# Performance work log

Hardware: AMD Instinct MI355X
Metric: run time of the kernel (lower is better)

## Reference

```python
import jax, jax.numpy as jnp
import numpy as np

N = 262144
IN_DIM = 1024
HID = 256
E = 16
TOP_K = 2


def setup_inputs() -> dict:
    key = jax.random.key(0)
    k1, k2, k3, k4, k5 = jax.random.split(key, 5)
    x = jax.random.normal(k1, (N, IN_DIM), dtype=jnp.float32)
    # Kaiming-ish init scaled for stability
    W1 = jax.random.normal(k2, (IN_DIM, HID), dtype=jnp.float32) * (1.0 / np.sqrt(IN_DIM))
    b1 = jnp.zeros((HID,), dtype=jnp.float32)
    W2 = jax.random.normal(k3, (HID, E), dtype=jnp.float32) * (1.0 / np.sqrt(HID))
    b2 = jnp.zeros((E,), dtype=jnp.float32)
    return {"x": x, "W1": W1, "b1": b1, "W2": W2, "b2": b2}


def reference(x, W1, b1, W2, b2):
    # MLP router: Linear -> ELU -> Linear
    h = jax.nn.elu(x @ W1 + b1)            # [N, HID]
    logits = h @ W2 + b2                   # [N, E]
    # top-k mask: keep top-k logits, set the rest to -inf (scatter semantics)
    vals, idx = jax.lax.top_k(logits, TOP_K)          # [N, K]
    rows = jnp.arange(logits.shape[0])[:, None]        # [N, 1]
    masked = jnp.full_like(logits, -jnp.inf).at[rows, idx].set(vals)
    alpha = jax.nn.softmax(masked, axis=-1)            # [N, E]
    return alpha, logits
```

## Files before the change

kernel.cpp:

```cpp
#include <hip/hip_runtime.h>
#include <math.h>

#define KDIM 1024
#define HID 256
#define NE 16
#define ROWS_BLK 64
#define KCH 32
#define NCHUNK 32
#define CH_BYTES 32768
#define W2T_PLANE (NE * HID)
#define BBASE 16384
#define BB_STRIDE 32768
#define SMEM_BYTES 81920

typedef __attribute__((ext_vector_type(4))) _Float16 f16x4;
typedef __attribute__((ext_vector_type(8))) _Float16 f16x8;
typedef __attribute__((ext_vector_type(16))) float f32x16;
typedef __attribute__((ext_vector_type(4))) float f32x4;

__device__ __forceinline__ void gld16(const void* g, void* s) {
  __builtin_amdgcn_global_load_lds(
      (const __attribute__((address_space(1))) void*)g,
      (__attribute__((address_space(3))) void*)s, 16, 0, 0);
}

__global__ void prep_w1(const float* __restrict__ W1, _Float16* __restrict__ img) {
  int idx = blockIdx.x * 256 + threadIdx.x;
  int col = idx & 255, kgl = idx >> 8;
  int c = kgl >> 2, kg = kgl & 3, k8 = kgl * 8;
  f16x8 p1, p2;
#pragma unroll
  for (int i = 0; i < 8; ++i) {
    float v = W1[(size_t)(k8 + i) * HID + col];
    _Float16 a = (_Float16)v;
    _Float16 b = (_Float16)((v - (float)a) * 4096.0f);
    p1[i] = a; p2[i] = b;
  }
  size_t off = (size_t)c * 16384 + (size_t)kg * 2048 + (size_t)col * 8;
  *(f16x8*)(img + off) = p1;
  *(f16x8*)(img + off + 8192) = p2;
}

__global__ void prep_w2(const float* __restrict__ W2, _Float16* __restrict__ w2t) {
  int idx = blockIdx.x * 256 + threadIdx.x;
  int e = idx & 15, k = idx >> 4;
  float v = W2[(size_t)k * NE + e];
  _Float16 a = (_Float16)v;
  _Float16 b = (_Float16)((v - (float)a) * 4096.0f);
  w2t[(size_t)e * HID + k] = a;
  w2t[W2T_PLANE + (size_t)e * HID + k] = b;
}

__global__ __launch_bounds__(512, 4) void fused_router(
    const float* __restrict__ x, const _Float16* __restrict__ w1img,
    const _Float16* __restrict__ w2t, const float* __restrict__ bias1,
    const float* __restrict__ bias2, float* __restrict__ outA,
    float* __restrict__ outL)
{
  extern __shared__ char smem[];
  const int t = threadIdx.x, l = t & 63, w = t >> 6;
  const int rowg = w >> 2, colg = w & 3;
  const int l31 = l & 31, hi = l >> 5;
  const int R0 = blockIdx.x * ROWS_BLK;
  const int arow = rowg * 32 + l31;
  const int bcol0 = colg * 64 + l31;

  const int xr = t >> 3, xq = t & 7;
  const float* xbase = x + (size_t)(R0 + xr) * KDIM + xq * 4;
  const int akg = xq >> 1, asub = (xq & 1) * 8;

  const char* ibase = (const char*)w1img + t * 16;

  f32x16 acc0[2], accA[2];
#pragma unroll
  for (int ct = 0; ct < 2; ++ct)
#pragma unroll
    for (int j = 0; j < 16; ++j) { acc0[ct][j] = 0.f; accA[ct][j] = 0.f; }

  float4 xv;

#define XLOAD(C_) do { xv = *(const float4*)(xbase + (size_t)(C_) * KCH); } while (0)

#define BSTAGE(C_, BS_) do {                                                  \
    const char* is_ = ibase + (size_t)(C_) * CH_BYTES;                        \
    char* bd_ = smem + BBASE + (BS_) * BB_STRIDE + t * 16;                    \
    gld16(is_,         bd_);                                                  \
    gld16(is_ + 8192,  bd_ + 8192);                                           \
    gld16(is_ + 16384, bd_ + 16384);                                          \
    gld16(is_ + 24576, bd_ + 24576);                                          \
  } while (0)

#define ASPLIT(BS_) do {                                                      \
    float vals_[4] = {xv.x, xv.y, xv.z, xv.w};                                \
    f16x4 pa_, pb_;                                                           \
    _Pragma("unroll") for (int j_ = 0; j_ < 4; ++j_) {                        \
      float v_ = vals_[j_];                                                   \
      _Float16 a_ = (_Float16)v_;                                             \
      _Float16 b_ = (_Float16)((v_ - (float)a_) * 4096.0f);                   \
      pa_[j_] = a_; pb_[j_] = b_;                                             \
    }                                                                         \
    int ao_ = (BS_) * 8192 + akg * 1024 + xr * 16 + asub;                     \
    *(f16x4*)(smem + ao_) = pa_;                                              \
    *(f16x4*)(smem + ao_ + 4096) = pb_;                                       \
  } while (0)

#define COMPUTE(BS_) do {                                                     \
    _Pragma("unroll") for (int s_ = 0; s_ < 2; ++s_) {                        \
      const int gg_ = 2 * s_ + hi;                                            \
      int ao_ = (BS_) * 8192 + gg_ * 1024 + arow * 16;                        \
      f16x8 a1_ = *(const f16x8*)(smem + ao_);                                \
      f16x8 a2_ = *(const f16x8*)(smem + ao_ + 4096);                         \
      _Pragma("unroll") for (int ct_ = 0; ct_ < 2; ++ct_) {                   \
        int bo_ = BBASE + (BS_) * BB_STRIDE + gg_ * 4096                      \
                  + (bcol0 + 32 * ct_) * 16;                                  \
        f16x8 b1_ = *(const f16x8*)(smem + bo_);                              \
        f16x8 b2_ = *(const f16x8*)(smem + bo_ + 16384);                      \
        acc0[ct_] = __builtin_amdgcn_mfma_f32_32x32x16_f16(                   \
            a1_, b1_, acc0[ct_], 0, 0, 0);                                    \
        accA[ct_] = __builtin_amdgcn_mfma_f32_32x32x16_f16(                   \
            a1_, b2_, accA[ct_], 0, 0, 0);                                    \
        accA[ct_] = __builtin_amdgcn_mfma_f32_32x32x16_f16(                   \
            a2_, b1_, accA[ct_], 0, 0, 0);                                    \
      }                                                                       \
    }                                                                         \
  } while (0)

  XLOAD(0);
  BSTAGE(0, 0);
  ASPLIT(0);
  XLOAD(1);
  __syncthreads();

  int bsel = 0;
#pragma unroll 1
  for (int c = 0; c < NCHUNK; ++c) {
    if (c + 1 < NCHUNK) {
      BSTAGE(c + 1, bsel ^ 1);
      ASPLIT(bsel ^ 1);
      if (c + 2 < NCHUNK) XLOAD(c + 2);
    }
    COMPUTE(bsel);
    __syncthreads();
    bsel ^= 1;
  }

  const float c12 = 1.0f / 4096.0f;
  const int tok = l & 15, g2 = l >> 4;

#pragma unroll
  for (int ct = 0; ct < 2; ++ct) {
    int col = bcol0 + 32 * ct;
    float bc = bias1[col];
    int cg = col >> 3, cb = (col & 7) * 2;
#pragma unroll
    for (int r = 0; r < 16; ++r) {
      int row = rowg * 32 + (r & 3) + 8 * (r >> 2) + 4 * hi;
      float v = acc0[ct][r] + c12 * accA[ct][r] + bc;
      v = v > 0.f ? v : expm1f(v);
      _Float16 h1 = (_Float16)v;
      _Float16 h2 = (_Float16)((v - (float)h1) * 4096.0f);
      int off = row * 512 + ((cg ^ (row & 7)) << 4) + cb;
      *(_Float16*)(smem + off) = h1;
      *(_Float16*)(smem + 32768 + off) = h2;
    }
  }
  __syncthreads();

  if (w < 4) {
    int tloc = w * 16 + tok;
    f32x4 L0, LA;
#pragma unroll
    for (int j = 0; j < 4; ++j) { L0[j] = 0.f; LA[j] = 0.f; }
    const _Float16* w2a = w2t + (size_t)tok * HID;
    const _Float16* w2b = w2a + W2T_PLANE;
#pragma unroll
    for (int kt = 0; kt < 8; ++kt) {
      int gg = (kt * 4 + g2) ^ (tloc & 7);
      f16x8 hb1 = *(const f16x8*)(smem + tloc * 512 + (gg << 4));
      f16x8 hb2 = *(const f16x8*)(smem + 32768 + tloc * 512 + (gg << 4));
      f16x8 wa = *(const f16x8*)(w2a + kt * 32 + 8 * g2);
      f16x8 wb = *(const f16x8*)(w2b + kt * 32 + 8 * g2);
      L0 = __builtin_amdgcn_mfma_f32_16x16x32_f16(wa, hb1, L0, 0, 0, 0);
      LA = __builtin_amdgcn_mfma_f32_16x16x32_f16(wa, hb2, LA, 0, 0, 0);
      LA = __builtin_amdgcn_mfma_f32_16x16x32_f16(wb, hb1, LA, 0, 0, 0);
    }
    float4 b2v = *(const float4*)(bias2 + 4 * g2);
    float L[4];
    L[0] = L0[0] + c12 * LA[0] + b2v.x;
    L[1] = L0[1] + c12 * LA[1] + b2v.y;
    L[2] = L0[2] + c12 * LA[2] + b2v.z;
    L[3] = L0[3] + c12 * LA[3] + b2v.w;

    float o1[4], o2[4], o3[4];
#pragma unroll
    for (int j = 0; j < 4; ++j) o1[j] = __shfl_xor(L[j], 16);
#pragma unroll
    for (int j = 0; j < 4; ++j) o2[j] = __shfl_xor(L[j], 32);
#pragma unroll
    for (int j = 0; j < 4; ++j) o3[j] = __shfl_xor(o1[j], 32);

    float all16[16];
#pragma unroll
    for (int cq = 0; cq < 4; ++cq) {
      int xg = cq ^ g2;
#pragma unroll
      for (int j = 0; j < 4; ++j) {
        float v = L[j];
        v = (xg == 1) ? o1[j] : v;
        v = (xg == 2) ? o2[j] : v;
        v = (xg == 3) ? o3[j] : v;
        all16[cq * 4 + j] = v;
      }
    }

    int i1 = 0; float m1 = all16[0];
#pragma unroll
    for (int e = 1; e < 16; ++e) { if (all16[e] > m1) { m1 = all16[e]; i1 = e; } }
    int i2 = -1; float m2 = -INFINITY;
#pragma unroll
    for (int e = 0; e < 16; ++e) { if (e != i1 && all16[e] > m2) { m2 = all16[e]; i2 = e; } }
    float ex = expf(m2 - m1);
    float sden = 1.f + ex;
    float A1 = 1.f / sden;
    float A2 = ex / sden;

    int e0 = 4 * g2;
    float4 alv;
    alv.x = (e0 + 0 == i1) ? A1 : ((e0 + 0 == i2) ? A2 : 0.f);
    alv.y = (e0 + 1 == i1) ? A1 : ((e0 + 1 == i2) ? A2 : 0.f);
    alv.z = (e0 + 2 == i1) ? A1 : ((e0 + 2 == i2) ? A2 : 0.f);
    alv.w = (e0 + 3 == i1) ? A1 : ((e0 + 3 == i2) ? A2 : 0.f);

    size_t orow = (size_t)(R0 + tloc);
    float4 lgv; lgv.x = L[0]; lgv.y = L[1]; lgv.z = L[2]; lgv.w = L[3];
    *(float4*)(outL + orow * NE + e0) = lgv;
    *(float4*)(outA + orow * NE + e0) = alv;
  }
#undef XLOAD
#undef BSTAGE
#undef ASPLIT
#undef COMPUTE
}

extern "C" void kernel_launch(void* const* d_in, const int* in_sizes, int n_in,
                              void* d_out, int out_size, void* d_ws, size_t ws_size,
                              hipStream_t stream) {
  const float* x  = (const float*)d_in[0];
  const float* W1 = (const float*)d_in[1];
  const float* b1 = (const float*)d_in[2];
  const float* W2 = (const float*)d_in[3];
  const float* b2 = (const float*)d_in[4];
  _Float16* w1img = (_Float16*)d_ws;
  _Float16* w2t = w1img + (size_t)NCHUNK * (CH_BYTES / 2);
  float* outA = (float*)d_out;
  const size_t n_tok = (size_t)in_sizes[0] / KDIM;
  float* outL = outA + n_tok * NE;

  prep_w1<<<dim3(128), dim3(256), 0, stream>>>(W1, w1img);
  prep_w2<<<dim3(16), dim3(256), 0, stream>>>(W2, w2t);

  hipFuncSetAttribute((const void*)fused_router,
                      hipFuncAttributeMaxDynamicSharedMemorySize, SMEM_BYTES);
  fused_router<<<dim3((unsigned)(n_tok / ROWS_BLK)), dim3(512), SMEM_BYTES, stream>>>(
      x, w1img, w2t, b1, b2, outA, outL);
}
```

Baseline: 575.6 us.

## Double rows per block to 128 so each staged W1 chunk is reused twice

Each block now processes 128 rows instead of 64, and every wave computes two 32-row MFMA tiles against the same B fragments. This halves W1 image staging per row and doubles B reuse from LDS. The cost is more accumulator registers (launch bounds lowered to 2 blocks per CU), larger LDS use, and half as many blocks. The epilogue now runs in two passes, one per 64-row half, with the extra barriers that requires.

```diff
diff --git a/kernel.cpp b/kernel.cpp
--- a/kernel.cpp
+++ b/kernel.cpp
@@ -4,16 +4,16 @@
 #define KDIM 1024
 #define HID 256
 #define NE 16
-#define ROWS_BLK 64
+#define ROWS_BLK 128
 #define KCH 32
 #define NCHUNK 32
 #define CH_BYTES 32768
 #define W2T_PLANE (NE * HID)
-#define BBASE 16384
+#define AB_STRIDE 16384
+#define BBASE 32768
 #define BB_STRIDE 32768
-#define SMEM_BYTES 81920
-
-typedef __attribute__((ext_vector_type(4))) _Float16 f16x4;
+#define SMEM_BYTES 98304
+
 typedef __attribute__((ext_vector_type(8))) _Float16 f16x8;
 typedef __attribute__((ext_vector_type(16))) float f32x16;
 typedef __attribute__((ext_vector_type(4))) float f32x4;
@@ -51,7 +51,7 @@
   w2t[W2T_PLANE + (size_t)e * HID + k] = b;
 }
 
-__global__ __launch_bounds__(512, 4) void fused_router(
+__global__ __launch_bounds__(512, 2) void fused_router(
     const float* __restrict__ x, const _Float16* __restrict__ w1img,
     const _Float16* __restrict__ w2t, const float* __restrict__ bias1,
     const float* __restrict__ bias2, float* __restrict__ outA,
@@ -62,24 +62,28 @@
   const int rowg = w >> 2, colg = w & 3;
   const int l31 = l & 31, hi = l >> 5;
   const int R0 = blockIdx.x * ROWS_BLK;
-  const int arow = rowg * 32 + l31;
+  const int arow0 = rowg * 64 + l31;
   const int bcol0 = colg * 64 + l31;
 
-  const int xr = t >> 3, xq = t & 7;
-  const float* xbase = x + (size_t)(R0 + xr) * KDIM + xq * 4;
-  const int akg = xq >> 1, asub = (xq & 1) * 8;
+  const int xr = t >> 2, xq = t & 3;
+  const float* xbase = x + (size_t)(R0 + xr) * KDIM + xq * 8;
 
   const char* ibase = (const char*)w1img + t * 16;
 
-  f32x16 acc0[2], accA[2];
-#pragma unroll
-  for (int ct = 0; ct < 2; ++ct)
-#pragma unroll
-    for (int j = 0; j < 16; ++j) { acc0[ct][j] = 0.f; accA[ct][j] = 0.f; }
-
-  float4 xv;
-
-#define XLOAD(C_) do { xv = *(const float4*)(xbase + (size_t)(C_) * KCH); } while (0)
+  f32x16 acc0[2][2], accA[2][2];
+#pragma unroll
+  for (int rt = 0; rt < 2; ++rt)
+#pragma unroll
+    for (int ct = 0; ct < 2; ++ct)
+#pragma unroll
+      for (int j = 0; j < 16; ++j) { acc0[rt][ct][j] = 0.f; accA[rt][ct][j] = 0.f; }
+
+  float xv[8];
+
+#define XLOAD(C_) do {                                                        \
+    *(float4*)(xv)     = *(const float4*)(xbase + (size_t)(C_) * KCH);       \
+    *(float4*)(xv + 4) = *(const float4*)(xbase + (size_t)(C_) * KCH + 4);   \
+  } while (0)
 
 #define BSTAGE(C_, BS_) do {                                                  \
     const char* is_ = ibase + (size_t)(C_) * CH_BYTES;                        \
@@ -91,36 +95,40 @@
   } while (0)
 
 #define ASPLIT(BS_) do {                                                      \
-    float vals_[4] = {xv.x, xv.y, xv.z, xv.w};                                \
-    f16x4 pa_, pb_;                                                           \
-    _Pragma("unroll") for (int j_ = 0; j_ < 4; ++j_) {                        \
-      float v_ = vals_[j_];                                                   \
+    f16x8 pa_, pb_;                                                           \
+    _Pragma("unroll") for (int j_ = 0; j_ < 8; ++j_) {                        \
+      float v_ = xv[j_];                                                      \
       _Float16 a_ = (_Float16)v_;                                             \
       _Float16 b_ = (_Float16)((v_ - (float)a_) * 4096.0f);                   \
       pa_[j_] = a_; pb_[j_] = b_;                                             \
     }                                                                         \
-    int ao_ = (BS_) * 8192 + akg * 1024 + xr * 16 + asub;                     \
-    *(f16x4*)(smem + ao_) = pa_;                                              \
-    *(f16x4*)(smem + ao_ + 4096) = pb_;                                       \
+    int ao_ = (BS_) * AB_STRIDE + xq * 2048 + xr * 16;                        \
+    *(f16x8*)(smem + ao_) = pa_;                                              \
+    *(f16x8*)(smem + ao_ + 8192) = pb_;                                       \
   } while (0)
 
 #define COMPUTE(BS_) do {                                                     \
     _Pragma("unroll") for (int s_ = 0; s_ < 2; ++s_) {                        \
       const int gg_ = 2 * s_ + hi;                                            \
-      int ao_ = (BS_) * 8192 + gg_ * 1024 + arow * 16;                        \
-      f16x8 a1_ = *(const f16x8*)(smem + ao_);                                \
-      f16x8 a2_ = *(const f16x8*)(smem + ao_ + 4096);                         \
+      f16x8 a1_[2], a2_[2];                                                   \
+      _Pragma("unroll") for (int rt_ = 0; rt_ < 2; ++rt_) {                   \
+        int ao_ = (BS_) * AB_STRIDE + gg_ * 2048 + (arow0 + 32 * rt_) * 16;   \
+        a1_[rt_] = *(const f16x8*)(smem + ao_);                               \
+        a2_[rt_] = *(const f16x8*)(smem + ao_ + 8192);                        \
+      }                                                                       \
       _Pragma("unroll") for (int ct_ = 0; ct_ < 2; ++ct_) {                   \
         int bo_ = BBASE + (BS_) * BB_STRIDE + gg_ * 4096                      \
                   + (bcol0 + 32 * ct_) * 16;                                  \
         f16x8 b1_ = *(const f16x8*)(smem + bo_);                              \
         f16x8 b2_ = *(const f16x8*)(smem + bo_ + 16384);                      \
-        acc0[ct_] = __builtin_amdgcn_mfma_f32_32x32x16_f16(                   \
-            a1_, b1_, acc0[ct_], 0, 0, 0);                                    \
-        accA[ct_] = __builtin_amdgcn_mfma_f32_32x32x16_f16(                   \
-            a1_, b2_, accA[ct_], 0, 0, 0);                                    \
-        accA[ct_] = __builtin_amdgcn_mfma_f32_32x32x16_f16(                   \
-            a2_, b1_, accA[ct_], 0, 0, 0);                                    \
+        _Pragma("unroll") for (int rt_ = 0; rt_ < 2; ++rt_) {                 \
+          acc0[rt_][ct_] = __builtin_amdgcn_mfma_f32_32x32x16_f16(            \
+              a1_[rt_], b1_, acc0[rt_][ct_], 0, 0, 0);                        \
+          accA[rt_][ct_] = __builtin_amdgcn_mfma_f32_32x32x16_f16(            \
+              a1_[rt_], b2_, accA[rt_][ct_], 0, 0, 0);                        \
+          accA[rt_][ct_] = __builtin_amdgcn_mfma_f32_32x32x16_f16(            \
+              a2_[rt_], b1_, accA[rt_][ct_], 0, 0, 0);                        \
+        }                                                                     \
       }                                                                       \
     }                                                                         \
   } while (0)
@@ -147,94 +155,102 @@
   const float c12 = 1.0f / 4096.0f;
   const int tok = l & 15, g2 = l >> 4;
 
-#pragma unroll
-  for (int ct = 0; ct < 2; ++ct) {
-    int col = bcol0 + 32 * ct;
-    float bc = bias1[col];
-    int cg = col >> 3, cb = (col & 7) * 2;
-#pragma unroll
-    for (int r = 0; r < 16; ++r) {
-      int row = rowg * 32 + (r & 3) + 8 * (r >> 2) + 4 * hi;
-      float v = acc0[ct][r] + c12 * accA[ct][r] + bc;
-      v = v > 0.f ? v : expm1f(v);
-      _Float16 h1 = (_Float16)v;
-      _Float16 h2 = (_Float16)((v - (float)h1) * 4096.0f);
-      int off = row * 512 + ((cg ^ (row & 7)) << 4) + cb;
-      *(_Float16*)(smem + off) = h1;
-      *(_Float16*)(smem + 32768 + off) = h2;
-    }
-  }
-  __syncthreads();
-
-  if (w < 4) {
-    int tloc = w * 16 + tok;
-    f32x4 L0, LA;
-#pragma unroll
-    for (int j = 0; j < 4; ++j) { L0[j] = 0.f; LA[j] = 0.f; }
-    const _Float16* w2a = w2t + (size_t)tok * HID;
-    const _Float16* w2b = w2a + W2T_PLANE;
-#pragma unroll
-    for (int kt = 0; kt < 8; ++kt) {
-      int gg = (kt * 4 + g2) ^ (tloc & 7);
-      f16x8 hb1 = *(const f16x8*)(smem + tloc * 512 + (gg << 4));
-      f16x8 hb2 = *(const f16x8*)(smem + 32768 + tloc * 512 + (gg << 4));
-      f16x8 wa = *(const f16x8*)(w2a + kt * 32 + 8 * g2);
-      f16x8 wb = *(const f16x8*)(w2b + kt * 32 + 8 * g2);
-      L0 = __builtin_amdgcn_mfma_f32_16x16x32_f16(wa, hb1, L0, 0, 0, 0);
-      LA = __builtin_amdgcn_mfma_f32_16x16x32_f16(wa, hb2, LA, 0, 0, 0);
-      LA = __builtin_amdgcn_mfma_f32_16x16x32_f16(wb, hb1, LA, 0, 0, 0);
-    }
-    float4 b2v = *(const float4*)(bias2 + 4 * g2);
-    float L[4];
-    L[0] = L0[0] + c12 * LA[0] + b2v.x;
-    L[1] = L0[1] + c12 * LA[1] + b2v.y;
-    L[2] = L0[2] + c12 * LA[2] + b2v.z;
-    L[3] = L0[3] + c12 * LA[3] + b2v.w;
-
-    float o1[4], o2[4], o3[4];
-#pragma unroll
-    for (int j = 0; j < 4; ++j) o1[j] = __shfl_xor(L[j], 16);
-#pragma unroll
-    for (int j = 0; j < 4; ++j) o2[j] = __shfl_xor(L[j], 32);
-#pragma unroll
-    for (int j = 0; j < 4; ++j) o3[j] = __shfl_xor(o1[j], 32);
-
-    float all16[16];
-#pragma unroll
-    for (int cq = 0; cq < 4; ++cq) {
-      int xg = cq ^ g2;
-#pragma unroll
-      for (int j = 0; j < 4; ++j) {
-        float v = L[j];
-        v = (xg == 1) ? o1[j] : v;
-        v = (xg == 2) ? o2[j] : v;
-        v = (xg == 3) ? o3[j] : v;
-        all16[cq * 4 + j] = v;
+#pragma unroll 1
+  for (int p = 0; p < 2; ++p) {
+    __syncthreads();
+    if (rowg == p) {
+#pragma unroll
+      for (int ct = 0; ct < 2; ++ct) {
+        int col = bcol0 + 32 * ct;
+        float bc = bias1[col];
+        int cg = col >> 3, cb = (col & 7) * 2;
+#pragma unroll
+        for (int rt = 0; rt < 2; ++rt) {
+#pragma unroll
+          for (int r = 0; r < 16; ++r) {
+            int tloc = 32 * rt + (r & 3) + 8 * (r >> 2) + 4 * hi;
+            float v = acc0[rt][ct][r] + c12 * accA[rt][ct][r] + bc;
+            v = v > 0.f ? v : expm1f(v);
+            _Float16 h1 = (_Float16)v;
+            _Float16 h2 = (_Float16)((v - (float)h1) * 4096.0f);
+            int off = tloc * 512 + ((cg ^ (tloc & 7)) << 4) + cb;
+            *(_Float16*)(smem + off) = h1;
+            *(_Float16*)(smem + 32768 + off) = h2;
+          }
+        }
       }
     }
-
-    int i1 = 0; float m1 = all16[0];
-#pragma unroll
-    for (int e = 1; e < 16; ++e) { if (all16[e] > m1) { m1 = all16[e]; i1 = e; } }
-    int i2 = -1; float m2 = -INFINITY;
-#pragma unroll
-    for (int e = 0; e < 16; ++e) { if (e != i1 && all16[e] > m2) { m2 = all16[e]; i2 = e; } }
-    float ex = expf(m2 - m1);
-    float sden = 1.f + ex;
-    float A1 = 1.f / sden;
-    float A2 = ex / sden;
-
-    int e0 = 4 * g2;
-    float4 alv;
-    alv.x = (e0 + 0 == i1) ? A1 : ((e0 + 0 == i2) ? A2 : 0.f);
-    alv.y = (e0 + 1 == i1) ? A1 : ((e0 + 1 == i2) ? A2 : 0.f);
-    alv.z = (e0 + 2 == i1) ? A1 : ((e0 + 2 == i2) ? A2 : 0.f);
-    alv.w = (e0 + 3 == i1) ? A1 : ((e0 + 3 == i2) ? A2 : 0.f);
-
-    size_t orow = (size_t)(R0 + tloc);
-    float4 lgv; lgv.x = L[0]; lgv.y = L[1]; lgv.z = L[2]; lgv.w = L[3];
-    *(float4*)(outL + orow * NE + e0) = lgv;
-    *(float4*)(outA + orow * NE + e0) = alv;
+    __syncthreads();
+    if (w < 4) {
+      int tloc = w * 16 + tok;
+      f32x4 L0, LA;
+#pragma unroll
+      for (int j = 0; j < 4; ++j) { L0[j] = 0.f; LA[j] = 0.f; }
+      const _Float16* w2a = w2t + (size_t)tok * HID;
+      const _Float16* w2b = w2a + W2T_PLANE;
+#pragma unroll
+      for (int kt = 0; kt < 8; ++kt) {
+        int gg = (kt * 4 + g2) ^ (tloc & 7);
+        f16x8 hb1 = *(const f16x8*)(smem + tloc * 512 + (gg << 4));
+        f16x8 hb2 = *(const f16x8*)(smem + 32768 + tloc * 512 + (gg << 4));
+        f16x8 wa = *(const f16x8*)(w2a + kt * 32 + 8 * g2);
+        f16x8 wb = *(const f16x8*)(w2b + kt * 32 + 8 * g2);
+        L0 = __builtin_amdgcn_mfma_f32_16x16x32_f16(wa, hb1, L0, 0, 0, 0);
+        LA = __builtin_amdgcn_mfma_f32_16x16x32_f16(wa, hb2, LA, 0, 0, 0);
+        LA = __builtin_amdgcn_mfma_f32_16x16x32_f16(wb, hb1, LA, 0, 0, 0);
+      }
+      float4 b2v = *(const float4*)(bias2 + 4 * g2);
+      float L[4];
+      L[0] = L0[0] + c12 * LA[0] + b2v.x;
+      L[1] = L0[1] + c12 * LA[1] + b2v.y;
+      L[2] = L0[2] + c12 * LA[2] + b2v.z;
+      L[3] = L0[3] + c12 * LA[3] + b2v.w;
+
+      float o1[4], o2[4], o3[4];
+#pragma unroll
+      for (int j = 0; j < 4; ++j) o1[j] = __shfl_xor(L[j], 16);
+#pragma unroll
+      for (int j = 0; j < 4; ++j) o2[j] = __shfl_xor(L[j], 32);
+#pragma unroll
+      for (int j = 0; j < 4; ++j) o3[j] = __shfl_xor(o1[j], 32);
+
+      float all16[16];
+#pragma unroll
+      for (int cq = 0; cq < 4; ++cq) {
+        int xg = cq ^ g2;
+#pragma unroll
+        for (int j = 0; j < 4; ++j) {
+          float v = L[j];
+          v = (xg == 1) ? o1[j] : v;
+          v = (xg == 2) ? o2[j] : v;
+          v = (xg == 3) ? o3[j] : v;
+          all16[cq * 4 + j] = v;
+        }
+      }
+
+      int i1 = 0; float m1 = all16[0];
+#pragma unroll
+      for (int e = 1; e < 16; ++e) { if (all16[e] > m1) { m1 = all16[e]; i1 = e; } }
+      int i2 = -1; float m2 = -INFINITY;
+#pragma unroll
+      for (int e = 0; e < 16; ++e) { if (e != i1 && all16[e] > m2) { m2 = all16[e]; i2 = e; } }
+      float ex = expf(m2 - m1);
+      float sden = 1.f + ex;
+      float A1 = 1.f / sden;
+      float A2 = ex / sden;
+
+      int e0 = 4 * g2;
+      float4 alv;
+      alv.x = (e0 + 0 == i1) ? A1 : ((e0 + 0 == i2) ? A2 : 0.f);
+      alv.y = (e0 + 1 == i1) ? A1 : ((e0 + 1 == i2) ? A2 : 0.f);
+      alv.z = (e0 + 2 == i1) ? A1 : ((e0 + 2 == i2) ? A2 : 0.f);
+      alv.w = (e0 + 3 == i1) ? A1 : ((e0 + 3 == i2) ? A2 : 0.f);
+
+      size_t orow = (size_t)(R0 + p * 64 + tloc);
+      float4 lgv; lgv.x = L[0]; lgv.y = L[1]; lgv.z = L[2]; lgv.w = L[3];
+      *(float4*)(outL + orow * NE + e0) = lgv;
+      *(float4*)(outA + orow * NE + e0) = alv;
+    }
   }
 #undef XLOAD
 #undef BSTAGE
```

Result: slower. 601.1 us (+4.4%).

## Deepen main-loop pipeline to 4-stage LDS ring with register-prefetched fragments

Applied to the files above, without the earlier changes.

Replaces the double-buffered K loop with a 4-slot LDS ring for A and B, staging two chunks ahead and loading x three chunks ahead. Fragments for the next half-chunk are read into registers while the MFMAs for the current one run, with explicit waitcnt and raw s_barrier replacing __syncthreads. MFMA issue is raised with setprio. SMEM grows to 160KB and launch bounds drop to 2 blocks per CU, which cuts occupancy and could limit latency hiding at the block level.

```diff
diff --git a/kernel.cpp b/kernel.cpp
--- a/kernel.cpp
+++ b/kernel.cpp
@@ -9,14 +9,16 @@
 #define NCHUNK 32
 #define CH_BYTES 32768
 #define W2T_PLANE (NE * HID)
-#define BBASE 16384
-#define BB_STRIDE 32768
-#define SMEM_BYTES 81920
+#define ABUF(i) (((i) & 3) * 8192)
+#define BBUF(i) (32768 + ((i) & 3) * 32768)
+#define SMEM_BYTES 163840
 
 typedef __attribute__((ext_vector_type(4))) _Float16 f16x4;
 typedef __attribute__((ext_vector_type(8))) _Float16 f16x8;
 typedef __attribute__((ext_vector_type(16))) float f32x16;
 typedef __attribute__((ext_vector_type(4))) float f32x4;
+
+struct Frag6 { f16x8 a1, a2, b1c0, b2c0, b1c1, b2c1; };
 
 __device__ __forceinline__ void gld16(const void* g, void* s) {
   __builtin_amdgcn_global_load_lds(
@@ -51,7 +53,7 @@
   w2t[W2T_PLANE + (size_t)e * HID + k] = b;
 }
 
-__global__ __launch_bounds__(512, 4) void fused_router(
+__global__ __launch_bounds__(512, 2) void fused_router(
     const float* __restrict__ x, const _Float16* __restrict__ w1img,
     const _Float16* __restrict__ w2t, const float* __restrict__ bias1,
     const float* __restrict__ bias2, float* __restrict__ outA,
@@ -77,21 +79,22 @@
 #pragma unroll
     for (int j = 0; j < 16; ++j) { acc0[ct][j] = 0.f; accA[ct][j] = 0.f; }
 
-  float4 xv;
-
-#define XLOAD(C_) do { xv = *(const float4*)(xbase + (size_t)(C_) * KCH); } while (0)
-
-#define BSTAGE(C_, BS_) do {                                                  \
+  float4 xv0, xv1;
+  Frag6 fA, fB;
+
+#define XLOADV(XV_, C_) do { XV_ = *(const float4*)(xbase + (size_t)(C_) * KCH); } while (0)
+
+#define BSTAGE(C_) do {                                                       \
     const char* is_ = ibase + (size_t)(C_) * CH_BYTES;                        \
-    char* bd_ = smem + BBASE + (BS_) * BB_STRIDE + t * 16;                    \
+    char* bd_ = smem + BBUF(C_) + t * 16;                                     \
     gld16(is_,         bd_);                                                  \
     gld16(is_ + 8192,  bd_ + 8192);                                           \
     gld16(is_ + 16384, bd_ + 16384);                                          \
     gld16(is_ + 24576, bd_ + 24576);                                          \
   } while (0)
 
-#define ASPLIT(BS_) do {                                                      \
-    float vals_[4] = {xv.x, xv.y, xv.z, xv.w};                                \
+#define ASPLITV(XV_, C_) do {                                                 \
+    float vals_[4] = {(XV_).x, (XV_).y, (XV_).z, (XV_).w};                    \
     f16x4 pa_, pb_;                                                           \
     _Pragma("unroll") for (int j_ = 0; j_ < 4; ++j_) {                        \
       float v_ = vals_[j_];                                                   \
@@ -99,54 +102,77 @@
       _Float16 b_ = (_Float16)((v_ - (float)a_) * 4096.0f);                   \
       pa_[j_] = a_; pb_[j_] = b_;                                             \
     }                                                                         \
-    int ao_ = (BS_) * 8192 + akg * 1024 + xr * 16 + asub;                     \
+    int ao_ = ABUF(C_) + akg * 1024 + xr * 16 + asub;                         \
     *(f16x4*)(smem + ao_) = pa_;                                              \
     *(f16x4*)(smem + ao_ + 4096) = pb_;                                       \
   } while (0)
 
-#define COMPUTE(BS_) do {                                                     \
-    _Pragma("unroll") for (int s_ = 0; s_ < 2; ++s_) {                        \
-      const int gg_ = 2 * s_ + hi;                                            \
-      int ao_ = (BS_) * 8192 + gg_ * 1024 + arow * 16;                        \
-      f16x8 a1_ = *(const f16x8*)(smem + ao_);                                \
-      f16x8 a2_ = *(const f16x8*)(smem + ao_ + 4096);                         \
-      _Pragma("unroll") for (int ct_ = 0; ct_ < 2; ++ct_) {                   \
-        int bo_ = BBASE + (BS_) * BB_STRIDE + gg_ * 4096                      \
-                  + (bcol0 + 32 * ct_) * 16;                                  \
-        f16x8 b1_ = *(const f16x8*)(smem + bo_);                              \
-        f16x8 b2_ = *(const f16x8*)(smem + bo_ + 16384);                      \
-        acc0[ct_] = __builtin_amdgcn_mfma_f32_32x32x16_f16(                   \
-            a1_, b1_, acc0[ct_], 0, 0, 0);                                    \
-        accA[ct_] = __builtin_amdgcn_mfma_f32_32x32x16_f16(                   \
-            a1_, b2_, accA[ct_], 0, 0, 0);                                    \
-        accA[ct_] = __builtin_amdgcn_mfma_f32_32x32x16_f16(                   \
-            a2_, b1_, accA[ct_], 0, 0, 0);                                    \
-      }                                                                       \
-    }                                                                         \
-  } while (0)
-
-  XLOAD(0);
-  BSTAGE(0, 0);
-  ASPLIT(0);
-  XLOAD(1);
-  __syncthreads();
-
-  int bsel = 0;
+#define FRAG6(F_, C_, S_) do {                                                \
+    const int gg_ = 2 * (S_) + hi;                                            \
+    int ao_ = ABUF(C_) + gg_ * 1024 + arow * 16;                              \
+    (F_).a1 = *(const f16x8*)(smem + ao_);                                    \
+    (F_).a2 = *(const f16x8*)(smem + ao_ + 4096);                             \
+    int bo_ = BBUF(C_) + gg_ * 4096 + bcol0 * 16;                             \
+    (F_).b1c0 = *(const f16x8*)(smem + bo_);                                  \
+    (F_).b2c0 = *(const f16x8*)(smem + bo_ + 16384);                          \
+    (F_).b1c1 = *(const f16x8*)(smem + bo_ + 512);                            \
+    (F_).b2c1 = *(const f16x8*)(smem + bo_ + 16384 + 512);                    \
+  } while (0)
+
+#define MFMA6(F_) do {                                                        \
+    __builtin_amdgcn_s_setprio(1);                                            \
+    acc0[0] = __builtin_amdgcn_mfma_f32_32x32x16_f16((F_).a1, (F_).b1c0, acc0[0], 0, 0, 0); \
+    accA[0] = __builtin_amdgcn_mfma_f32_32x32x16_f16((F_).a1, (F_).b2c0, accA[0], 0, 0, 0); \
+    accA[0] = __builtin_amdgcn_mfma_f32_32x32x16_f16((F_).a2, (F_).b1c0, accA[0], 0, 0, 0); \
+    acc0[1] = __builtin_amdgcn_mfma_f32_32x32x16_f16((F_).a1, (F_).b1c1, acc0[1], 0, 0, 0); \
+    accA[1] = __builtin_amdgcn_mfma_f32_32x32x16_f16((F_).a1, (F_).b2c1, accA[1], 0, 0, 0); \
+    accA[1] = __builtin_amdgcn_mfma_f32_32x32x16_f16((F_).a2, (F_).b1c1, accA[1], 0, 0, 0); \
+    __builtin_amdgcn_s_setprio(0);                                            \
+  } while (0)
+
+#define BODY(C_, FCUR_, FNXT_, XSP_, XLD_, STG_, XL_, LA_, VMSTR_) do {       \
+    if (STG_) { BSTAGE((C_) + 2); ASPLITV(XSP_, (C_) + 2); }                  \
+    __builtin_amdgcn_sched_barrier(0);              \
+    if (XL_) XLOADV(XLD_, (C_) + 3);                                          \
+    Frag6 fs1_; FRAG6(fs1_, (C_), 1);                                         \
+    MFMA6(FCUR_);                                                             \
+    if (LA_) FRAG6(FNXT_, (C_) + 1, 0);                                       \
+    MFMA6(fs1_);                                                              \
+    __builtin_amdgcn_sched_barrier(0);                                        \
+    asm volatile("s_waitcnt vmcnt(" VMSTR_ ")" ::: "memory");                 \
+    asm volatile("s_waitcnt lgkmcnt(6)" ::: "memory");                        \
+    __builtin_amdgcn_sched_barrier(0);                                        \
+    __builtin_amdgcn_s_barrier();                                             \
+  } while (0)
+
+  XLOADV(xv0, 0);
+  XLOADV(xv1, 1);
+  BSTAGE(0);
+  BSTAGE(1);
+  ASPLITV(xv0, 0);
+  ASPLITV(xv1, 1);
+  XLOADV(xv0, 2);
+  __builtin_amdgcn_sched_barrier(0);
+  asm volatile("s_waitcnt vmcnt(1)" ::: "memory");
+  asm volatile("s_waitcnt lgkmcnt(0)" ::: "memory");
+  __builtin_amdgcn_sched_barrier(0);
+  __builtin_amdgcn_s_barrier();
+  FRAG6(fA, 0, 0);
+
 #pragma unroll 1
-  for (int c = 0; c < NCHUNK; ++c) {
-    if (c + 1 < NCHUNK) {
-      BSTAGE(c + 1, bsel ^ 1);
-      ASPLIT(bsel ^ 1);
-      if (c + 2 < NCHUNK) XLOAD(c + 2);
-    }
-    COMPUTE(bsel);
-    __syncthreads();
-    bsel ^= 1;
-  }
+  for (int cb = 0; cb < NCHUNK - 4; cb += 2) {
+    BODY(cb,     fA, fB, xv0, xv1, 1, 1, 1, "1");
+    BODY(cb + 1, fB, fA, xv1, xv0, 1, 1, 1, "1");
+  }
+  BODY(28, fA, fB, xv0, xv1, 1, 1, 1, "1");
+  BODY(29, fB, fA, xv1, xv0, 1, 0, 1, "0");
+  BODY(30, fA, fB, xv0, xv1, 0, 0, 1, "0");
+  BODY(31, fB, fA, xv1, xv0, 0, 0, 0, "0");
 
   const float c12 = 1.0f / 4096.0f;
   const int tok = l & 15, g2 = l >> 4;
 
+  __syncthreads();
 #pragma unroll
   for (int ct = 0; ct < 2; ++ct) {
     int col = bcol0 + 32 * ct;
@@ -154,12 +180,12 @@
     int cg = col >> 3, cb = (col & 7) * 2;
 #pragma unroll
     for (int r = 0; r < 16; ++r) {
-      int row = rowg * 32 + (r & 3) + 8 * (r >> 2) + 4 * hi;
+      int tloc = rowg * 32 + (r & 3) + 8 * (r >> 2) + 4 * hi;
       float v = acc0[ct][r] + c12 * accA[ct][r] + bc;
       v = v > 0.f ? v : expm1f(v);
       _Float16 h1 = (_Float16)v;
       _Float16 h2 = (_Float16)((v - (float)h1) * 4096.0f);
-      int off = row * 512 + ((cg ^ (row & 7)) << 4) + cb;
+      int off = tloc * 512 + ((cg ^ (tloc & 7)) << 4) + cb;
       *(_Float16*)(smem + off) = h1;
       *(_Float16*)(smem + 32768 + off) = h2;
     }
@@ -236,10 +262,12 @@
     *(float4*)(outL + orow * NE + e0) = lgv;
     *(float4*)(outA + orow * NE + e0) = alv;
   }
-#undef XLOAD
+#undef XLOADV
 #undef BSTAGE
-#undef ASPLIT
-#undef COMPUTE
+#undef ASPLITV
+#undef FRAG6
+#undef MFMA6
+#undef BODY
 }
 
 extern "C" void kernel_launch(void* const* d_in, const int* in_sizes, int n_in,
```

Result: slower. 734.1 us (+27.5%).

## Halve rows per block to 32 and give each wave one 32-column tile

Applied to the files above, without the earlier changes.

Each block now processes 32 rows instead of 64. Each of the 8 waves owns a single 32x32 output tile across all 256 hidden columns, instead of a 2-row-group by 4-column-group split with two tiles per wave. LDS use shrinks, only half the threads convert x to split fp16, and setprio is raised around the MFMA groups. The trade-off is that each W1 chunk staged in LDS is reused by only 32 rows, which doubles the number of blocks and the total W1 traffic.

```diff
diff --git a/kernel.cpp b/kernel.cpp
--- a/kernel.cpp
+++ b/kernel.cpp
@@ -4,16 +4,16 @@
 #define KDIM 1024
 #define HID 256
 #define NE 16
-#define ROWS_BLK 64
+#define ROWS_BLK 32
 #define KCH 32
 #define NCHUNK 32
 #define CH_BYTES 32768
 #define W2T_PLANE (NE * HID)
-#define BBASE 16384
+#define ABUF(i) ((i) * 4096)
+#define BBASE 8192
 #define BB_STRIDE 32768
-#define SMEM_BYTES 81920
-
-typedef __attribute__((ext_vector_type(4))) _Float16 f16x4;
+#define SMEM_BYTES 73728
+
 typedef __attribute__((ext_vector_type(8))) _Float16 f16x8;
 typedef __attribute__((ext_vector_type(16))) float f32x16;
 typedef __attribute__((ext_vector_type(4))) float f32x4;
@@ -59,23 +59,19 @@
 {
   extern __shared__ char smem[];
   const int t = threadIdx.x, l = t & 63, w = t >> 6;
-  const int rowg = w >> 2, colg = w & 3;
   const int l31 = l & 31, hi = l >> 5;
   const int R0 = blockIdx.x * ROWS_BLK;
-  const int arow = rowg * 32 + l31;
-  const int bcol0 = colg * 64 + l31;
-
-  const int xr = t >> 3, xq = t & 7;
+  const int bcol = w * 32 + l31;
+
+  const int xr = (t >> 3) & 31, xq = t & 7;
   const float* xbase = x + (size_t)(R0 + xr) * KDIM + xq * 4;
   const int akg = xq >> 1, asub = (xq & 1) * 8;
 
   const char* ibase = (const char*)w1img + t * 16;
 
-  f32x16 acc0[2], accA[2];
-#pragma unroll
-  for (int ct = 0; ct < 2; ++ct)
-#pragma unroll
-    for (int j = 0; j < 16; ++j) { acc0[ct][j] = 0.f; accA[ct][j] = 0.f; }
+  f32x16 acc0, accA;
+#pragma unroll
+  for (int j = 0; j < 16; ++j) { acc0[j] = 0.f; accA[j] = 0.f; }
 
   float4 xv;
 
@@ -91,37 +87,35 @@
   } while (0)
 
 #define ASPLIT(BS_) do {                                                      \
-    float vals_[4] = {xv.x, xv.y, xv.z, xv.w};                                \
-    f16x4 pa_, pb_;                                                           \
-    _Pragma("unroll") for (int j_ = 0; j_ < 4; ++j_) {                        \
-      float v_ = vals_[j_];                                                   \
-      _Float16 a_ = (_Float16)v_;                                             \
-      _Float16 b_ = (_Float16)((v_ - (float)a_) * 4096.0f);                   \
-      pa_[j_] = a_; pb_[j_] = b_;                                             \
+    if (t < 256) {                                                            \
+      float vals_[4] = {xv.x, xv.y, xv.z, xv.w};                              \
+      _Float16 pa_[4], pb_[4];                                                \
+      _Pragma("unroll") for (int j_ = 0; j_ < 4; ++j_) {                      \
+        float v_ = vals_[j_];                                                 \
+        _Float16 a_ = (_Float16)v_;                                           \
+        _Float16 b_ = (_Float16)((v_ - (float)a_) * 4096.0f);                 \
+        pa_[j_] = a_; pb_[j_] = b_;                                           \
+      }                                                                       \
+      int ao_ = ABUF(BS_) + akg * 512 + xr * 16 + asub;                       \
+      *(unsigned long long*)(smem + ao_) = *(unsigned long long*)pa_;         \
+      *(unsigned long long*)(smem + ao_ + 2048) = *(unsigned long long*)pb_;  \
     }                                                                         \
-    int ao_ = (BS_) * 8192 + akg * 1024 + xr * 16 + asub;                     \
-    *(f16x4*)(smem + ao_) = pa_;                                              \
-    *(f16x4*)(smem + ao_ + 4096) = pb_;                                       \
   } while (0)
 
 #define COMPUTE(BS_) do {                                                     \
     _Pragma("unroll") for (int s_ = 0; s_ < 2; ++s_) {                        \
       const int gg_ = 2 * s_ + hi;                                            \
-      int ao_ = (BS_) * 8192 + gg_ * 1024 + arow * 16;                        \
+      int ao_ = ABUF(BS_) + gg_ * 512 + l31 * 16;                             \
       f16x8 a1_ = *(const f16x8*)(smem + ao_);                                \
-      f16x8 a2_ = *(const f16x8*)(smem + ao_ + 4096);                         \
-      _Pragma("unroll") for (int ct_ = 0; ct_ < 2; ++ct_) {                   \
-        int bo_ = BBASE + (BS_) * BB_STRIDE + gg_ * 4096                      \
-                  + (bcol0 + 32 * ct_) * 16;                                  \
-        f16x8 b1_ = *(const f16x8*)(smem + bo_);                              \
-        f16x8 b2_ = *(const f16x8*)(smem + bo_ + 16384);                      \
-        acc0[ct_] = __builtin_amdgcn_mfma_f32_32x32x16_f16(                   \
-            a1_, b1_, acc0[ct_], 0, 0, 0);                                    \
-        accA[ct_] = __builtin_amdgcn_mfma_f32_32x32x16_f16(                   \
-            a1_, b2_, accA[ct_], 0, 0, 0);                                    \
-        accA[ct_] = __builtin_amdgcn_mfma_f32_32x32x16_f16(                   \
-            a2_, b1_, accA[ct_], 0, 0, 0);                                    \
-      }                                                                       \
+      f16x8 a2_ = *(const f16x8*)(smem + ao_ + 2048);                         \
+      int bo_ = BBASE + (BS_) * BB_STRIDE + gg_ * 4096 + bcol * 16;           \
+      f16x8 b1_ = *(const f16x8*)(smem + bo_);                                \
+      f16x8 b2_ = *(const f16x8*)(smem + bo_ + 16384);                        \
+      __builtin_amdgcn_s_setprio(1);                                          \
+      acc0 = __builtin_amdgcn_mfma_f32_32x32x16_f16(a1_, b1_, acc0, 0, 0, 0); \
+      accA = __builtin_amdgcn_mfma_f32_32x32x16_f16(a1_, b2_, accA, 0, 0, 0); \
+      accA = __builtin_amdgcn_mfma_f32_32x32x16_f16(a2_, b1_, accA, 0, 0, 0); \
+      __builtin_amdgcn_s_setprio(0);                                          \
     }                                                                         \
   } while (0)
 
@@ -147,26 +141,25 @@
   const float c12 = 1.0f / 4096.0f;
   const int tok = l & 15, g2 = l >> 4;
 
-#pragma unroll
-  for (int ct = 0; ct < 2; ++ct) {
-    int col = bcol0 + 32 * ct;
-    float bc = bias1[col];
-    int cg = col >> 3, cb = (col & 7) * 2;
+  __syncthreads();
+  {
+    float bc = bias1[bcol];
+    int cg = bcol >> 3, cb = (bcol & 7) * 2;
 #pragma unroll
     for (int r = 0; r < 16; ++r) {
-      int row = rowg * 32 + (r & 3) + 8 * (r >> 2) + 4 * hi;
-      float v = acc0[ct][r] + c12 * accA[ct][r] + bc;
+      int tloc = (r & 3) + 8 * (r >> 2) + 4 * hi;
+      float v = acc0[r] + c12 * accA[r] + bc;
       v = v > 0.f ? v : expm1f(v);
       _Float16 h1 = (_Float16)v;
       _Float16 h2 = (_Float16)((v - (float)h1) * 4096.0f);
-      int off = row * 512 + ((cg ^ (row & 7)) << 4) + cb;
+      int off = tloc * 512 + ((cg ^ (tloc & 7)) << 4) + cb;
       *(_Float16*)(smem + off) = h1;
-      *(_Float16*)(smem + 32768 + off) = h2;
+      *(_Float16*)(smem + 16384 + off) = h2;
     }
   }
   __syncthreads();
 
-  if (w < 4) {
+  if (w < 2) {
     int tloc = w * 16 + tok;
     f32x4 L0, LA;
 #pragma unroll
@@ -177,7 +170,7 @@
     for (int kt = 0; kt < 8; ++kt) {
       int gg = (kt * 4 + g2) ^ (tloc & 7);
       f16x8 hb1 = *(const f16x8*)(smem + tloc * 512 + (gg << 4));
-      f16x8 hb2 = *(const f16x8*)(smem + 32768 + tloc * 512 + (gg << 4));
+      f16x8 hb2 = *(const f16x8*)(smem + 16384 + tloc * 512 + (gg << 4));
       f16x8 wa = *(const f16x8*)(w2a + kt * 32 + 8 * g2);
       f16x8 wb = *(const f16x8*)(w2b + kt * 32 + 8 * g2);
       L0 = __builtin_amdgcn_mfma_f32_16x16x32_f16(wa, hb1, L0, 0, 0, 0);
```

Result: slower. 748.7 us (+30.1%).
